# Performance work log

Measured on AMD Instinct MI355X. Metric: run time of the kernel, lower is better.

The kernel has to match this reference:

```python
import jax, jax.numpy as jnp
import numpy as np

_MIN_BLOCK_KV = 32


def setup_inputs() -> dict:
    key = jax.random.key(0)
    k0, k1, k2, k3 = jax.random.split(key, 4)
    B, H, HKV, D, T, S = 32, 32, 8, 128, 2048, 8
    pool = B * T
    q = jax.random.normal(k0, (B, H, D), dtype=jnp.float32)
    k_buffer = jax.random.normal(k1, (pool, HKV, D), dtype=jnp.float32)
    v_buffer = jax.random.normal(k2, (pool, HKV, D), dtype=jnp.float32)
    # uniform contexts: request b owns tokens [b*T, (b+1)*T) of the pool, in permuted (paged) order
    kv_indptr = (jnp.arange(B + 1, dtype=jnp.int32) * T)
    kv_indices = jax.random.permutation(k3, pool).astype(jnp.int32)
    num_kv_splits = jnp.full((B,), S, dtype=jnp.int32)
    return {"q": q, "k_buffer": k_buffer, "v_buffer": v_buffer,
            "kv_indptr": kv_indptr, "kv_indices": kv_indices,
            "num_kv_splits": num_kv_splits}


def reference(q, k_buffer, v_buffer, kv_indptr, kv_indices, num_kv_splits):
    # Paged KV-cache decode attention, stage 1 (split-KV partial softmax).
    B, H, D = q.shape
    HKV = k_buffer.shape[1]
    Lv = v_buffer.shape[-1]
    G = H // HKV                       # GQA group size
    sm_scale = 1.0 / (D ** 0.5)        # Model default (sm_scale=None)
    logit_cap = 0.0                    # Model default -> capping disabled

    seq_lens = kv_indptr[1:] - kv_indptr[:-1]          # [B]
    T = kv_indices.shape[0] // B                       # max context len (uniform setup)
    S = int(jnp.max(num_kv_splits))                    # max_kv_splits (eager, as in torch code)

    pos = jnp.arange(T, dtype=jnp.int32)               # [T]
    valid = pos[None, :] < seq_lens[:, None]           # [B,T]
    # gather KV pool locations per (batch, position); clamp OOB positions
    gidx = kv_indptr[:-1, None] + jnp.minimum(pos[None, :], seq_lens[:, None] - 1)
    kv_loc = kv_indices[gidx]                          # [B,T]
    k_g = k_buffer[kv_loc]                             # [B,T,HKV,D]
    v_g = v_buffer[kv_loc]                             # [B,T,HKV,Lv]

    qr = q.reshape(B, HKV, G, D)
    qk = jnp.einsum('bkgd,btkd->bkgt', qr, k_g) * sm_scale   # [B,HKV,G,T]
    if logit_cap > 0:
        qk = logit_cap * jnp.tanh(qk / logit_cap)

    # split assignment: kv_len_per_split = cdiv(cdiv(seq_len, splits), MIN) * MIN
    cdiv = lambda a, b: (a + b - 1) // b
    kv_len_per_split = cdiv(cdiv(seq_lens, num_kv_splits), _MIN_BLOCK_KV) * _MIN_BLOCK_KV  # [B]
    split_id = pos[None, :] // kv_len_per_split[:, None]      # [B,T]
    split_mask = (split_id[:, None, :] == jnp.arange(S, dtype=jnp.int32)[None, :, None]) \
                 & valid[:, None, :]                          # [B,S,T]

    neg_inf = jnp.float32(-jnp.inf)
    masked = jnp.where(split_mask[:, None, None, :, :], qk[:, :, :, None, :], neg_inf)  # [B,HKV,G,S,T]
    m = jnp.max(masked, axis=-1)                               # [B,HKV,G,S]
    m_safe = jnp.where(jnp.isfinite(m), m, 0.0)                # guard empty splits
    p = jnp.exp(masked - m_safe[..., None])                    # [B,HKV,G,S,T]
    p = jnp.where(split_mask[:, None, None, :, :], p, 0.0)
    e_sum = jnp.sum(p, axis=-1)                                # [B,HKV,G,S]
    acc = jnp.einsum('bkgst,btkv->bkgsv', p, v_g)              # [B,HKV,G,S,Lv]

    att_out = (acc / e_sum[..., None]).reshape(B, H, S, Lv)
    att_lse = (m + jnp.log(e_sum)).reshape(B, H, S)
    return att_out, att_lse
```

## Files before the change

### kernel.cpp

```cpp
#include <hip/hip_runtime.h>
#include <math.h>


namespace {
constexpr int kB = 32;
constexpr int kH = 32;
constexpr int kHKV = 8;
constexpr int kD = 128;
constexpr int kG = kH / kHKV;
constexpr int kS = 8;
constexpr int kMinBlockKV = 32;
}

__global__ __launch_bounds__(256, 4) void decode_split_kernel(
    const float* __restrict__ q,
    const float* __restrict__ k_buffer,
    const float* __restrict__ v_buffer,
    const int* __restrict__ kv_indptr,
    const int* __restrict__ kv_indices,
    const int* __restrict__ num_kv_splits,
    float* __restrict__ att_out,
    float* __restrict__ att_lse)
{
    const int bid = blockIdx.x;
    const int s  = bid % kS;
    const int kh = (bid / kS) % kHKV;
    const int b  = bid / (kS * kHKV);

    const int tid  = threadIdx.x;
    const int wave = tid >> 6;
    const int lane = tid & 63;
    const int tg   = lane >> 4;
    const int li   = lane & 15;

    const int ptr0    = kv_indptr[b];
    const int seq_len = kv_indptr[b + 1] - ptr0;
    const int splits  = num_kv_splits[b];
    const int per     = (seq_len + splits - 1) / splits;
    const int lps     = ((per + kMinBlockKV - 1) / kMinBlockKV) * kMinBlockKV;
    const int t0 = s * lps;
    const int t1 = min(t0 + lps, seq_len);

    const float sm_scale = 0.08838834764831845f;

    float4 q0[kG], q1[kG];
    const float* qb = q + ((size_t)b * kH + (size_t)kh * kG) * kD;
    #pragma unroll
    for (int g = 0; g < kG; ++g) {
        float4 a = *(const float4*)(qb + (size_t)g * kD + li * 4);
        float4 c = *(const float4*)(qb + (size_t)g * kD + 64 + li * 4);
        q0[g] = make_float4(a.x * sm_scale, a.y * sm_scale, a.z * sm_scale, a.w * sm_scale);
        q1[g] = make_float4(c.x * sm_scale, c.y * sm_scale, c.z * sm_scale, c.w * sm_scale);
    }

    float  l[kG] = {0.f, 0.f, 0.f, 0.f};
    float4 a0[kG], a1[kG];
    #pragma unroll
    for (int g = 0; g < kG; ++g) {
        a0[g] = make_float4(0.f, 0.f, 0.f, 0.f);
        a1[g] = make_float4(0.f, 0.f, 0.f, 0.f);
    }

    if (t1 - t0 == 256) {
        const int base = t0 + wave * 64;
        const int my_loc = kv_indices[ptr0 + base + lane];

        int loc = __shfl(my_loc, tg);
        const float* kb = k_buffer + ((size_t)loc * kHKV + kh) * kD;
        const float* vb = v_buffer + ((size_t)loc * kHKV + kh) * kD;
        float4 ck0 = *(const float4*)(kb + li * 4);
        float4 ck1 = *(const float4*)(kb + 64 + li * 4);
        float4 cv0 = *(const float4*)(vb + li * 4);
        float4 cv1 = *(const float4*)(vb + 64 + li * 4);

        #pragma unroll
        for (int ig = 0; ig < 16; ++ig) {
            const int nidx = (ig < 15) ? ((ig + 1) * 4 + tg) : tg;
            const int loc2 = __shfl(my_loc, nidx);
            const float* kb2 = k_buffer + ((size_t)loc2 * kHKV + kh) * kD;
            const float* vb2 = v_buffer + ((size_t)loc2 * kHKV + kh) * kD;
            const float4 nk0 = *(const float4*)(kb2 + li * 4);
            const float4 nk1 = *(const float4*)(kb2 + 64 + li * 4);
            const float4 nv0 = *(const float4*)(vb2 + li * 4);
            const float4 nv1 = *(const float4*)(vb2 + 64 + li * 4);

            float dot[kG];
            #pragma unroll
            for (int g = 0; g < kG; ++g) {
                float d = q0[g].x * ck0.x;
                d = fmaf(q0[g].y, ck0.y, d);
                d = fmaf(q0[g].z, ck0.z, d);
                d = fmaf(q0[g].w, ck0.w, d);
                d = fmaf(q1[g].x, ck1.x, d);
                d = fmaf(q1[g].y, ck1.y, d);
                d = fmaf(q1[g].z, ck1.z, d);
                d = fmaf(q1[g].w, ck1.w, d);
                dot[g] = d;
            }
            #pragma unroll
            for (int m = 1; m <= 8; m <<= 1) {
                #pragma unroll
                for (int g = 0; g < kG; ++g)
                    dot[g] += __shfl_xor(dot[g], m);
            }
            #pragma unroll
            for (int g = 0; g < kG; ++g) {
                const float p = __expf(dot[g]);
                l[g] += p;
                a0[g].x = fmaf(p, cv0.x, a0[g].x);
                a0[g].y = fmaf(p, cv0.y, a0[g].y);
                a0[g].z = fmaf(p, cv0.z, a0[g].z);
                a0[g].w = fmaf(p, cv0.w, a0[g].w);
                a1[g].x = fmaf(p, cv1.x, a1[g].x);
                a1[g].y = fmaf(p, cv1.y, a1[g].y);
                a1[g].z = fmaf(p, cv1.z, a1[g].z);
                a1[g].w = fmaf(p, cv1.w, a1[g].w);
            }
            ck0 = nk0; ck1 = nk1; cv0 = nv0; cv1 = nv1;
        }
    } else {
        for (int base = t0 + wave * 64; base < t1; base += 256) {
            const int nt = min(64, t1 - base);
            int my_loc = 0;
            if (lane < nt) my_loc = kv_indices[ptr0 + base + lane];
            const int ng = (nt + 3) >> 2;

            for (int ig = 0; ig < ng; ++ig) {
                const int idx = ig * 4 + tg;
                const int loc = __shfl(my_loc, min(idx, nt - 1));
                const float* kb = k_buffer + ((size_t)loc * kHKV + kh) * kD;
                const float* vb = v_buffer + ((size_t)loc * kHKV + kh) * kD;
                const float4 ck0 = *(const float4*)(kb + li * 4);
                const float4 ck1 = *(const float4*)(kb + 64 + li * 4);
                const float4 cv0 = *(const float4*)(vb + li * 4);
                const float4 cv1 = *(const float4*)(vb + 64 + li * 4);

                float dot[kG];
                #pragma unroll
                for (int g = 0; g < kG; ++g) {
                    float d = q0[g].x * ck0.x;
                    d = fmaf(q0[g].y, ck0.y, d);
                    d = fmaf(q0[g].z, ck0.z, d);
                    d = fmaf(q0[g].w, ck0.w, d);
                    d = fmaf(q1[g].x, ck1.x, d);
                    d = fmaf(q1[g].y, ck1.y, d);
                    d = fmaf(q1[g].z, ck1.z, d);
                    d = fmaf(q1[g].w, ck1.w, d);
                    dot[g] = d;
                }
                #pragma unroll
                for (int m = 1; m <= 8; m <<= 1) {
                    #pragma unroll
                    for (int g = 0; g < kG; ++g)
                        dot[g] += __shfl_xor(dot[g], m);
                }
                const bool valid = idx < nt;
                #pragma unroll
                for (int g = 0; g < kG; ++g) {
                    const float p = valid ? __expf(dot[g]) : 0.f;
                    l[g] += p;
                    a0[g].x = fmaf(p, cv0.x, a0[g].x);
                    a0[g].y = fmaf(p, cv0.y, a0[g].y);
                    a0[g].z = fmaf(p, cv0.z, a0[g].z);
                    a0[g].w = fmaf(p, cv0.w, a0[g].w);
                    a1[g].x = fmaf(p, cv1.x, a1[g].x);
                    a1[g].y = fmaf(p, cv1.y, a1[g].y);
                    a1[g].z = fmaf(p, cv1.z, a1[g].z);
                    a1[g].w = fmaf(p, cv1.w, a1[g].w);
                }
            }
        }
    }

    #pragma unroll
    for (int m = 16; m <= 32; m <<= 1) {
        #pragma unroll
        for (int g = 0; g < kG; ++g) {
            a0[g].x += __shfl_xor(a0[g].x, m);
            a0[g].y += __shfl_xor(a0[g].y, m);
            a0[g].z += __shfl_xor(a0[g].z, m);
            a0[g].w += __shfl_xor(a0[g].w, m);
            a1[g].x += __shfl_xor(a1[g].x, m);
            a1[g].y += __shfl_xor(a1[g].y, m);
            a1[g].z += __shfl_xor(a1[g].z, m);
            a1[g].w += __shfl_xor(a1[g].w, m);
            l[g] += __shfl_xor(l[g], m);
        }
    }

    __shared__ float s_acc[4][kG][kD];
    __shared__ float s_l[4][kG];
    if (tg == 0) {
        #pragma unroll
        for (int g = 0; g < kG; ++g) {
            *(float4*)&s_acc[wave][g][li * 4]      = a0[g];
            *(float4*)&s_acc[wave][g][64 + li * 4] = a1[g];
        }
        if (li == 0) {
            #pragma unroll
            for (int g = 0; g < kG; ++g) s_l[wave][g] = l[g];
        }
    }
    __syncthreads();

    const int g = tid >> 6;
    const int d = (tid & 63) * 2;
    float o0 = 0.f, o1 = 0.f, ls = 0.f;
    #pragma unroll
    for (int w = 0; w < 4; ++w) {
        o0 += s_acc[w][g][d];
        o1 += s_acc[w][g][d + 1];
        ls += s_l[w][g];
    }
    const float inv = 1.0f / ls;
    const size_t hidx = (size_t)b * kH + (size_t)kh * kG + g;
    float* outp = att_out + (hidx * kS + s) * kD + d;
    outp[0] = o0 * inv;
    outp[1] = o1 * inv;
    if ((tid & 63) == 0)
        att_lse[hidx * kS + s] = logf(ls);
}

extern "C" void kernel_launch(void* const* d_in, const int* in_sizes, int n_in,
                              void* d_out, int out_size, void* d_ws, size_t ws_size,
                              hipStream_t stream) {
    const float* q             = (const float*)d_in[0];
    const float* k_buffer      = (const float*)d_in[1];
    const float* v_buffer      = (const float*)d_in[2];
    const int*   kv_indptr     = (const int*)d_in[3];
    const int*   kv_indices    = (const int*)d_in[4];
    const int*   num_kv_splits = (const int*)d_in[5];

    float* att_out = (float*)d_out;
    float* att_lse = att_out + (size_t)kB * kH * kS * kD;

    dim3 grid(kB * kHKV * kS);
    decode_split_kernel<<<grid, 256, 0, stream>>>(
        q, k_buffer, v_buffer, kv_indptr, kv_indices, num_kv_splits,
        att_out, att_lse);
}
```

Measured before the change: 570.2 us.

## Stage paged KV rows via async global-to-LDS loads with double buffering and DPP reductions

The fast path now issues direct global-to-LDS loads (global_load_lds, 16 bytes per lane) into a per-wave two-slot ring and prefetches two chunks ahead. Explicit vmcnt waits gate each slot before it is read back from LDS. The 16-lane dot-product reduction switches from shfl_xor to DPP row operations in both paths, and the reduction scratch reuses the ring buffer. The aim is to overlap gather latency with compute and cut cross-lane shuffle cost, at the price of 32KB of LDS per block, which may lower occupancy, plus hand-coded waitcnt values that are fragile.

New measurement: 630.9 us. 1.11x slower.

```diff
diff --git a/kernel.cpp b/kernel.cpp
--- a/kernel.cpp
+++ b/kernel.cpp
@@ -10,6 +10,26 @@
 constexpr int kG = kH / kHKV;
 constexpr int kS = 8;
 constexpr int kMinBlockKV = 32;
+}
+
+template<int CTRL>
+__device__ __forceinline__ float dpp_add(float x) {
+    int t = __builtin_amdgcn_update_dpp(0, __float_as_int(x), CTRL, 0xF, 0xF, true);
+    return x + __int_as_float(t);
+}
+
+__device__ __forceinline__ float row16_sum(float x) {
+    x = dpp_add<0xB1>(x);
+    x = dpp_add<0x4E>(x);
+    x = dpp_add<0x141>(x);
+    x = dpp_add<0x140>(x);
+    return x;
+}
+
+__device__ __forceinline__ void load_lds16(const float* g, float* lds) {
+    __builtin_amdgcn_global_load_lds(
+        (const __attribute__((address_space(1))) void*)g,
+        (__attribute__((address_space(3))) void*)lds, 16, 0, 0);
 }
 
 __global__ __launch_bounds__(256, 4) void decode_split_kernel(
@@ -61,30 +81,43 @@
         a1[g] = make_float4(0.f, 0.f, 0.f, 0.f);
     }
 
+    __shared__ __align__(16) float ring[4][2][1024];
+
     if (t1 - t0 == 256) {
-        const int base = t0 + wave * 64;
+        const int base   = t0 + wave * 64;
         const int my_loc = kv_indices[ptr0 + base + lane];
-
-        int loc = __shfl(my_loc, tg);
-        const float* kb = k_buffer + ((size_t)loc * kHKV + kh) * kD;
-        const float* vb = v_buffer + ((size_t)loc * kHKV + kh) * kD;
-        float4 ck0 = *(const float4*)(kb + li * 4);
-        float4 ck1 = *(const float4*)(kb + 64 + li * 4);
-        float4 cv0 = *(const float4*)(vb + li * 4);
-        float4 cv1 = *(const float4*)(vb + 64 + li * 4);
+        const int sub = lane >> 5;
+        const int col = (lane & 31) * 4;
+
+        auto issue = [&](int c) {
+            const int loc01 = __shfl(my_loc, c * 4 + sub);
+            const int loc23 = __shfl(my_loc, c * 4 + 2 + sub);
+            const float* k01 = k_buffer + ((size_t)loc01 * kHKV + kh) * kD + col;
+            const float* k23 = k_buffer + ((size_t)loc23 * kHKV + kh) * kD + col;
+            const float* v01 = v_buffer + ((size_t)loc01 * kHKV + kh) * kD + col;
+            const float* v23 = v_buffer + ((size_t)loc23 * kHKV + kh) * kD + col;
+            float* slot = &ring[wave][c & 1][0];
+            load_lds16(k01, slot);
+            load_lds16(k23, slot + 256);
+            load_lds16(v01, slot + 512);
+            load_lds16(v23, slot + 768);
+        };
+
+        issue(0);
+        issue(1);
 
         #pragma unroll
-        for (int ig = 0; ig < 16; ++ig) {
-            const int nidx = (ig < 15) ? ((ig + 1) * 4 + tg) : tg;
-            const int loc2 = __shfl(my_loc, nidx);
-            const float* kb2 = k_buffer + ((size_t)loc2 * kHKV + kh) * kD;
-            const float* vb2 = v_buffer + ((size_t)loc2 * kHKV + kh) * kD;
-            const float4 nk0 = *(const float4*)(kb2 + li * 4);
-            const float4 nk1 = *(const float4*)(kb2 + 64 + li * 4);
-            const float4 nv0 = *(const float4*)(vb2 + li * 4);
-            const float4 nv1 = *(const float4*)(vb2 + 64 + li * 4);
-
-            float dot[kG];
+        for (int c = 0; c < 16; ++c) {
+            if (c < 15) __builtin_amdgcn_s_waitcnt(0xF74);
+            else        __builtin_amdgcn_s_waitcnt(0xF70);
+            asm volatile("" ::: "memory");
+
+            const float* slot = &ring[wave][c & 1][0];
+            const float4 ck0 = *(const float4*)(slot + tg * 128 + li * 4);
+            const float4 ck1 = *(const float4*)(slot + tg * 128 + 64 + li * 4);
+            const float4 cv0 = *(const float4*)(slot + 512 + tg * 128 + li * 4);
+            const float4 cv1 = *(const float4*)(slot + 512 + tg * 128 + 64 + li * 4);
+
             #pragma unroll
             for (int g = 0; g < kG; ++g) {
                 float d = q0[g].x * ck0.x;
@@ -95,17 +128,8 @@
                 d = fmaf(q1[g].y, ck1.y, d);
                 d = fmaf(q1[g].z, ck1.z, d);
                 d = fmaf(q1[g].w, ck1.w, d);
-                dot[g] = d;
-            }
-            #pragma unroll
-            for (int m = 1; m <= 8; m <<= 1) {
-                #pragma unroll
-                for (int g = 0; g < kG; ++g)
-                    dot[g] += __shfl_xor(dot[g], m);
-            }
-            #pragma unroll
-            for (int g = 0; g < kG; ++g) {
-                const float p = __expf(dot[g]);
+                d = row16_sum(d);
+                const float p = __expf(d);
                 l[g] += p;
                 a0[g].x = fmaf(p, cv0.x, a0[g].x);
                 a0[g].y = fmaf(p, cv0.y, a0[g].y);
@@ -116,7 +140,11 @@
                 a1[g].z = fmaf(p, cv1.z, a1[g].z);
                 a1[g].w = fmaf(p, cv1.w, a1[g].w);
             }
-            ck0 = nk0; ck1 = nk1; cv0 = nv0; cv1 = nv1;
+
+            if (c + 2 < 16) {
+                asm volatile("" ::: "memory");
+                issue(c + 2);
+            }
         }
     } else {
         for (int base = t0 + wave * 64; base < t1; base += 256) {
@@ -135,7 +163,7 @@
                 const float4 cv0 = *(const float4*)(vb + li * 4);
                 const float4 cv1 = *(const float4*)(vb + 64 + li * 4);
 
-                float dot[kG];
+                const bool valid = idx < nt;
                 #pragma unroll
                 for (int g = 0; g < kG; ++g) {
                     float d = q0[g].x * ck0.x;
@@ -146,18 +174,8 @@
                     d = fmaf(q1[g].y, ck1.y, d);
                     d = fmaf(q1[g].z, ck1.z, d);
                     d = fmaf(q1[g].w, ck1.w, d);
-                    dot[g] = d;
-                }
-                #pragma unroll
-                for (int m = 1; m <= 8; m <<= 1) {
-                    #pragma unroll
-                    for (int g = 0; g < kG; ++g)
-                        dot[g] += __shfl_xor(dot[g], m);
-                }
-                const bool valid = idx < nt;
-                #pragma unroll
-                for (int g = 0; g < kG; ++g) {
-                    const float p = valid ? __expf(dot[g]) : 0.f;
+                    d = row16_sum(d);
+                    const float p = valid ? __expf(d) : 0.f;
                     l[g] += p;
                     a0[g].x = fmaf(p, cv0.x, a0[g].x);
                     a0[g].y = fmaf(p, cv0.y, a0[g].y);
@@ -188,17 +206,16 @@
         }
     }
 
-    __shared__ float s_acc[4][kG][kD];
-    __shared__ float s_l[4][kG];
+    float* comb = &ring[wave][0][0];
     if (tg == 0) {
         #pragma unroll
         for (int g = 0; g < kG; ++g) {
-            *(float4*)&s_acc[wave][g][li * 4]      = a0[g];
-            *(float4*)&s_acc[wave][g][64 + li * 4] = a1[g];
+            *(float4*)(comb + g * 128 + li * 4)      = a0[g];
+            *(float4*)(comb + g * 128 + 64 + li * 4) = a1[g];
         }
         if (li == 0) {
             #pragma unroll
-            for (int g = 0; g < kG; ++g) s_l[wave][g] = l[g];
+            for (int g = 0; g < kG; ++g) comb[512 + g] = l[g];
         }
     }
     __syncthreads();
@@ -208,9 +225,9 @@
     float o0 = 0.f, o1 = 0.f, ls = 0.f;
     #pragma unroll
     for (int w = 0; w < 4; ++w) {
-        o0 += s_acc[w][g][d];
-        o1 += s_acc[w][g][d + 1];
-        ls += s_l[w][g];
+        o0 += ring[w][0][g * 128 + d];
+        o1 += ring[w][0][g * 128 + d + 1];
+        ls += ring[w][0][512 + g];
     }
     const float inv = 1.0f / ls;
     const size_t hidx = (size_t)b * kH + (size_t)kh * kG + g;
```

## Use DPP row reductions, drop manual prefetch, raise occupancy, reorder block mapping

Applied to the files above, without the earlier changes.

Replaces the ds_bpermute-based shfl_xor reductions of the 16-lane dot products with DPP row operations (quad-permute and row shifts), which avoid LDS traffic. It removes the manual one-step software prefetch of K/V in the full-split path and raises the launch bound to 8 blocks per CU, relying on higher occupancy rather than in-thread prefetch to hide gather latency. The block index mapping now puts kv-head innermost, so neighbouring blocks share the same split and token indices. The risk is less latency hiding per wave if the compiler cannot fit eight blocks per CU, and correctness depends on the DPP row-shift sequence giving a full 16-lane sum in every lane.

Result: slower. 785.5 us (+37.7%).

```diff
diff --git a/kernel.cpp b/kernel.cpp
--- a/kernel.cpp
+++ b/kernel.cpp
@@ -12,7 +12,21 @@
 constexpr int kMinBlockKV = 32;
 }
 
-__global__ __launch_bounds__(256, 4) void decode_split_kernel(
+template<int CTRL>
+__device__ __forceinline__ float dpp_add(float x) {
+    int t = __builtin_amdgcn_update_dpp(0, __float_as_int(x), CTRL, 0xF, 0xF, true);
+    return x + __int_as_float(t);
+}
+
+__device__ __forceinline__ float row16_sum(float x) {
+    x = dpp_add<0xB1>(x);
+    x = dpp_add<0x4E>(x);
+    x = dpp_add<0x141>(x);
+    x = dpp_add<0x140>(x);
+    return x;
+}
+
+__global__ __launch_bounds__(256, 8) void decode_split_kernel(
     const float* __restrict__ q,
     const float* __restrict__ k_buffer,
     const float* __restrict__ v_buffer,
@@ -23,9 +37,9 @@
     float* __restrict__ att_lse)
 {
     const int bid = blockIdx.x;
-    const int s  = bid % kS;
-    const int kh = (bid / kS) % kHKV;
-    const int b  = bid / (kS * kHKV);
+    const int kh = bid & 7;
+    const int s  = (bid >> 3) & 7;
+    const int b  = bid >> 6;
 
     const int tid  = threadIdx.x;
     const int wave = tid >> 6;
@@ -62,29 +76,19 @@
     }
 
     if (t1 - t0 == 256) {
-        const int base = t0 + wave * 64;
+        const int base   = t0 + wave * 64;
         const int my_loc = kv_indices[ptr0 + base + lane];
-
-        int loc = __shfl(my_loc, tg);
-        const float* kb = k_buffer + ((size_t)loc * kHKV + kh) * kD;
-        const float* vb = v_buffer + ((size_t)loc * kHKV + kh) * kD;
-        float4 ck0 = *(const float4*)(kb + li * 4);
-        float4 ck1 = *(const float4*)(kb + 64 + li * 4);
-        float4 cv0 = *(const float4*)(vb + li * 4);
-        float4 cv1 = *(const float4*)(vb + 64 + li * 4);
 
         #pragma unroll
         for (int ig = 0; ig < 16; ++ig) {
-            const int nidx = (ig < 15) ? ((ig + 1) * 4 + tg) : tg;
-            const int loc2 = __shfl(my_loc, nidx);
-            const float* kb2 = k_buffer + ((size_t)loc2 * kHKV + kh) * kD;
-            const float* vb2 = v_buffer + ((size_t)loc2 * kHKV + kh) * kD;
-            const float4 nk0 = *(const float4*)(kb2 + li * 4);
-            const float4 nk1 = *(const float4*)(kb2 + 64 + li * 4);
-            const float4 nv0 = *(const float4*)(vb2 + li * 4);
-            const float4 nv1 = *(const float4*)(vb2 + 64 + li * 4);
-
-            float dot[kG];
+            const int loc = __shfl(my_loc, ig * 4 + tg);
+            const float* kb = k_buffer + ((size_t)loc * kHKV + kh) * kD;
+            const float* vb = v_buffer + ((size_t)loc * kHKV + kh) * kD;
+            const float4 ck0 = *(const float4*)(kb + li * 4);
+            const float4 ck1 = *(const float4*)(kb + 64 + li * 4);
+            const float4 cv0 = *(const float4*)(vb + li * 4);
+            const float4 cv1 = *(const float4*)(vb + 64 + li * 4);
+
             #pragma unroll
             for (int g = 0; g < kG; ++g) {
                 float d = q0[g].x * ck0.x;
@@ -95,17 +99,8 @@
                 d = fmaf(q1[g].y, ck1.y, d);
                 d = fmaf(q1[g].z, ck1.z, d);
                 d = fmaf(q1[g].w, ck1.w, d);
-                dot[g] = d;
-            }
-            #pragma unroll
-            for (int m = 1; m <= 8; m <<= 1) {
-                #pragma unroll
-                for (int g = 0; g < kG; ++g)
-                    dot[g] += __shfl_xor(dot[g], m);
-            }
-            #pragma unroll
-            for (int g = 0; g < kG; ++g) {
-                const float p = __expf(dot[g]);
+                d = row16_sum(d);
+                const float p = __expf(d);
                 l[g] += p;
                 a0[g].x = fmaf(p, cv0.x, a0[g].x);
                 a0[g].y = fmaf(p, cv0.y, a0[g].y);
@@ -116,7 +111,6 @@
                 a1[g].z = fmaf(p, cv1.z, a1[g].z);
                 a1[g].w = fmaf(p, cv1.w, a1[g].w);
             }
-            ck0 = nk0; ck1 = nk1; cv0 = nv0; cv1 = nv1;
         }
     } else {
         for (int base = t0 + wave * 64; base < t1; base += 256) {
@@ -135,7 +129,7 @@
                 const float4 cv0 = *(const float4*)(vb + li * 4);
                 const float4 cv1 = *(const float4*)(vb + 64 + li * 4);
 
-                float dot[kG];
+                const bool valid = idx < nt;
                 #pragma unroll
                 for (int g = 0; g < kG; ++g) {
                     float d = q0[g].x * ck0.x;
@@ -146,18 +140,8 @@
                     d = fmaf(q1[g].y, ck1.y, d);
                     d = fmaf(q1[g].z, ck1.z, d);
                     d = fmaf(q1[g].w, ck1.w, d);
-                    dot[g] = d;
-                }
-                #pragma unroll
-                for (int m = 1; m <= 8; m <<= 1) {
-                    #pragma unroll
-                    for (int g = 0; g < kG; ++g)
-                        dot[g] += __shfl_xor(dot[g], m);
-                }
-                const bool valid = idx < nt;
-                #pragma unroll
-                for (int g = 0; g < kG; ++g) {
-                    const float p = valid ? __expf(dot[g]) : 0.f;
+                    d = row16_sum(d);
+                    const float p = valid ? __expf(d) : 0.f;
                     l[g] += p;
                     a0[g].x = fmaf(p, cv0.x, a0[g].x);
                     a0[g].y = fmaf(p, cv0.y, a0[g].y);
```
